# Performance work log

Hardware: AMD Instinct MI355X
Metric: run time of the kernel (lower is better)

## Reference

```python
import jax, jax.numpy as jnp
import numpy as np

EPS = 1e-5

def _ln(x, g, b):
    m = x.mean(-1, keepdims=True)
    v = jnp.var(x, axis=-1, keepdims=True)
    return (x - m) * jax.lax.rsqrt(v + EPS) * g + b

def _conv(x, w, b, stride=1, pad=1):
    y = jax.lax.conv_general_dilated(x, w, (stride, stride), [(pad, pad), (pad, pad)],
                                     dimension_numbers=('NCHW', 'OIHW', 'NCHW'))
    return y + b[None, :, None, None]

def _bn(x, g, b, m, v):
    # inference-mode BatchNorm2d
    inv = jax.lax.rsqrt(v + EPS)
    return (x - m[None, :, None, None]) * (g * inv)[None, :, None, None] + b[None, :, None, None]

def _sru_dir(u0, u1, u2, res, vf, vr, bf, br, reverse):
    # elementwise gated recurrence (SRU v2, identity activation, no dropout)
    def step(c, inp):
        a0, a1, a2, rx = inp
        f = jax.nn.sigmoid(a1 + vf * c + bf)
        c2 = f * c + (1.0 - f) * a0
        r = jax.nn.sigmoid(a2 + vr * c2 + br)
        return c2, r * c2 + (1.0 - r) * rx
    c0 = jnp.zeros_like(u0[0])
    _, hs = jax.lax.scan(step, c0, (u0, u1, u2, res), reverse=reverse)
    return hs

def _sru_layer(x, g, b, wp, w, vc, bias, k, h):
    # x: [L,B,n_in]; layer_norm on input, factored weight (projection), bidirectional
    xn = _ln(x, g, b)
    L, B, _ = xn.shape
    U = (xn @ wp) @ w                      # [L,B,2*k*h]
    U = U.reshape(L, B, 2, k, h)
    outs = []
    for d, rev in ((0, False), (1, True)):
        u = U[:, :, d]
        res = u[..., 3, :] if k == 4 else xn[..., d * h:(d + 1) * h]
        outs.append(_sru_dir(u[..., 0, :], u[..., 1, :], u[..., 2, :], res,
                             vc[d, 0], vc[d, 1], bias[d, 0], bias[d, 1], rev))
    return jnp.concatenate(outs, axis=-1)

def _forward(x, conv0_w, conv0_b, rconv1_w, rconv1_b, rbn1_g, rbn1_b, rbn1_m, rbn1_v,
             rconv2_w, rconv2_b, rbn2_g, rbn2_b, rbn2_m, rbn2_v,
             ln0_g, ln0_b, wproj0, w0, vc0, bias0, ln_g, ln_b, wproj, w, vc, bias,
             cln_g, cln_b, cls_w):
    H = 512
    h = _conv(x, conv0_w, conv0_b, stride=2)           # [B,32,F/2,T/2]
    for i in range(3):                                  # 3 residual blocks
        r = h
        h1 = jax.nn.relu(_bn(_conv(h, rconv1_w[i], rconv1_b[i]), rbn1_g[i], rbn1_b[i], rbn1_m[i], rbn1_v[i]))
        h2 = _bn(_conv(h1, rconv2_w[i], rconv2_b[i]), rbn2_g[i], rbn2_b[i], rbn2_m[i], rbn2_v[i])
        h = jax.nn.relu(h2 + r)
    Bb, C, Fr, Tt = h.shape
    s = h.reshape(Bb, C * Fr, Tt).transpose(2, 0, 1)   # [T,B,2048]
    s = _sru_layer(s, ln0_g, ln0_b, wproj0, w0, vc0, bias0, 4, H)  # layer 0: n_in != n_out -> k=4
    for i in range(3):                                  # layers 1..3: n_in == n_out -> k=3
        s = _sru_layer(s, ln_g[i], ln_b[i], wproj[i], w[i], vc[i], bias[i], 3, H)
    s = s.transpose(1, 0, 2)                            # [B,T,1024]
    s = _ln(s, cln_g, cln_b)
    return s @ cls_w                                    # [B,T,30]

def setup_inputs():
    key = jax.random.key(0)
    ks = iter(jax.random.split(key, 32))
    def nrm(shape, scale=1.0):
        return jax.random.normal(next(ks), shape, jnp.float32) * scale
    H, P, F2, D, hb = 512, 256, 2048, 1024, -2.0
    d = {}
    d['x'] = nrm((16, 1, 128, 2048))
    d['conv0_w'] = nrm((32, 1, 3, 3), (2.0 / 9) ** 0.5)
    d['conv0_b'] = jnp.zeros((32,))
    d['rconv1_w'] = nrm((3, 32, 32, 3, 3), (2.0 / (32 * 9)) ** 0.5)
    d['rconv1_b'] = jnp.zeros((3, 32))
    d['rbn1_g'] = jnp.ones((3, 32)); d['rbn1_b'] = jnp.zeros((3, 32))
    d['rbn1_m'] = nrm((3, 32), 0.1); d['rbn1_v'] = jnp.ones((3, 32))
    d['rconv2_w'] = nrm((3, 32, 32, 3, 3), (2.0 / (32 * 9)) ** 0.5)
    d['rconv2_b'] = jnp.zeros((3, 32))
    d['rbn2_g'] = 0.1 * jnp.ones((3, 32)); d['rbn2_b'] = jnp.zeros((3, 32))
    d['rbn2_m'] = nrm((3, 32), 0.1); d['rbn2_v'] = jnp.ones((3, 32))
    d['ln0_g'] = jnp.ones((F2,)); d['ln0_b'] = jnp.zeros((F2,))
    d['wproj0'] = nrm((F2, P), F2 ** -0.5)
    d['w0'] = nrm((P, 2 * 4 * H), P ** -0.5)
    d['vc0'] = nrm((2, 2, H), 0.1)
    d['bias0'] = jnp.zeros((2, 2, H)).at[:, 0].set(hb)
    d['ln_g'] = jnp.ones((3, D)); d['ln_b'] = jnp.zeros((3, D))
    d['wproj'] = nrm((3, D, P), D ** -0.5)
    d['w'] = nrm((3, P, 2 * 3 * H), P ** -0.5)
    d['vc'] = nrm((3, 2, 2, H), 0.1)
    d['bias'] = jnp.zeros((3, 2, 2, H)).at[:, :, 0].set(hb)
    d['cln_g'] = jnp.ones((D,)); d['cln_b'] = jnp.zeros((D,))
    d['cls_w'] = nrm((D, 30), D ** -0.5)
    return d

def reference(x, conv0_w, conv0_b, rconv1_w, rconv1_b, rbn1_g, rbn1_b, rbn1_m, rbn1_v,
              rconv2_w, rconv2_b, rbn2_g, rbn2_b, rbn2_m, rbn2_v,
              ln0_g, ln0_b, wproj0, w0, vc0, bias0, ln_g, ln_b, wproj, w, vc, bias,
              cln_g, cln_b, cls_w):
    return _forward(x, conv0_w, conv0_b, rconv1_w, rconv1_b, rbn1_g, rbn1_b, rbn1_m, rbn1_v,
                    rconv2_w, rconv2_b, rbn2_g, rbn2_b, rbn2_m, rbn2_v,
                    ln0_g, ln0_b, wproj0, w0, vc0, bias0, ln_g, ln_b, wproj, w, vc, bias,
                    cln_g, cln_b, cls_w)
```

## Files before the change

kernel.cpp:

```cpp
#include <hip/hip_runtime.h>
#include <hip/hip_bf16.h>
#include <math.h>

#define DEV __device__ __forceinline__

typedef __attribute__((ext_vector_type(8))) short short8;
typedef __attribute__((ext_vector_type(4))) float floatx4;

DEV float b2f_lo(unsigned u) { return __uint_as_float(u << 16); }
DEV float b2f_hi(unsigned u) { return __uint_as_float(u & 0xffff0000u); }

#if __has_builtin(__builtin_amdgcn_exp2f)
DEV float fexp2_(float x) { return __builtin_amdgcn_exp2f(x); }
#else
DEV float fexp2_(float x) { return exp2f(x); }
#endif
#if __has_builtin(__builtin_amdgcn_rcpf)
DEV float frcp_(float x) { return __builtin_amdgcn_rcpf(x); }
#else
DEV float frcp_(float x) { return 1.f / x; }
#endif

DEV void gl2lds16(const void* g, void* l) {
  __builtin_amdgcn_global_load_lds(
      (const __attribute__((address_space(1))) unsigned int*)g,
      (__attribute__((address_space(3))) unsigned int*)l, 16, 0, 0);
}

union U8 { uint4 u; __hip_bfloat16 h[8]; };

DEV int swz64(int x)    { return (x & ~63) | ((x & 15) << 2) | ((x >> 4) & 3); }
DEV int invswz64(int x) { return (x & ~63) | ((x & 3) << 4) | ((x >> 2) & 15); }

__global__ __launch_bounds__(256) void conv_stem_nhwc(const float* __restrict__ x,
    const float* __restrict__ w, const float* __restrict__ bias,
    __hip_bfloat16* __restrict__ out) {
  __shared__ float sX[3][2052];
  __shared__ float sW[288];
  __shared__ float sB[32];
  const int tid = threadIdx.x;
  const int f = blockIdx.x, n = blockIdx.y;
  const float* xb = x + (size_t)n * 262144;

  for (int i = tid; i < 1536; i += 256) {
    int r = i >> 9, c4 = i & 511;
    int fi = 2 * f - 1 + r;
    float4 v = {0.f, 0.f, 0.f, 0.f};
    if (fi >= 0 && fi < 128) v = *(const float4*)&xb[fi * 2048 + c4 * 4];
    sX[r][1 + c4 * 4 + 0] = v.x;
    sX[r][1 + c4 * 4 + 1] = v.y;
    sX[r][1 + c4 * 4 + 2] = v.z;
    sX[r][1 + c4 * 4 + 3] = v.w;
  }
  if (tid < 3) { sX[tid][0] = 0.f; sX[tid][2049] = 0.f; }
  for (int i = tid; i < 288; i += 256) sW[i] = w[i];
  if (tid < 32) sB[tid] = bias[tid];
  __syncthreads();

  float xv[4][9];
#pragma unroll
  for (int q = 0; q < 4; ++q) {
    int t = tid + q * 256;
#pragma unroll
    for (int r = 0; r < 3; ++r)
#pragma unroll
      for (int dc = 0; dc < 3; ++dc)
        xv[q][r * 3 + dc] = sX[r][2 * t + dc];
  }

  U8 ores[4][4];
#pragma unroll
  for (int ocq = 0; ocq < 4; ++ocq) {
#pragma unroll
    for (int oo = 0; oo < 8; ++oo) {
      float w9[9];
#pragma unroll
      for (int qq = 0; qq < 9; ++qq) w9[qq] = sW[(ocq * 8 + oo) * 9 + qq];
      float b0 = sB[ocq * 8 + oo];
#pragma unroll
      for (int q = 0; q < 4; ++q) {
        float acc = b0;
#pragma unroll
        for (int qq = 0; qq < 9; ++qq) acc = fmaf(w9[qq], xv[q][qq], acc);
        ores[ocq][q].h[oo] = __float2bfloat16(acc);
      }
    }
  }

#pragma unroll
  for (int q = 0; q < 4; ++q) {
    int t = tid + q * 256;
    uint4* dst = (uint4*)&out[(((size_t)n * 64 + f) * 1024 + t) * 32];
    dst[0] = ores[0][q].u;
    dst[1] = ores[1][q].u;
    dst[2] = ores[2][q].u;
    dst[3] = ores[3][q].u;
  }
}

__global__ __launch_bounds__(256) void wtap_conv6(const float* __restrict__ w1,
    const float* __restrict__ w2, __hip_bfloat16* __restrict__ out) {
  int i = blockIdx.x * 256 + threadIdx.x;
  if (i < 55296) {
    int b = i / 9216, r = i - b * 9216;
    int layer = b >> 1, which = b & 1;
    const float* src = (which ? w2 : w1) + layer * 9216;
    int tap = r >> 10, oc = (r >> 5) & 31, ic = r & 31;
    out[b * 9216 + r] = __float2bfloat16(src[(oc * 32 + ic) * 9 + tap]);
  }
}

template <int ADD>
__global__ __launch_bounds__(256) void conv_mfma(const __hip_bfloat16* __restrict__ Hin,
    const __hip_bfloat16* __restrict__ wt,
    const float* __restrict__ cb, const float* __restrict__ bg,
    const float* __restrict__ bb, const float* __restrict__ bm,
    const float* __restrict__ bv, __hip_bfloat16* Hres) {
  __shared__ __hip_bfloat16 sIn[6 * 66 * 40];
  __hip_bfloat16* sOut = sIn;
  const int tid = threadIdx.x;
  const int tb = blockIdx.x, fb = blockIdx.y, n = blockIdx.z;
  const int t0 = tb * 64, f0 = fb * 4;
  const __hip_bfloat16* Hb = Hin + (size_t)n * 2097152;

  for (int c = tid; c < 1584; c += 256) {
    int rr = c / 264;
    int r2 = c - rr * 264;
    int p = r2 >> 2, icq = r2 & 3;
    int fi = f0 - 1 + rr;
    int tg = t0 + p - 1;
    uint4 v = {0, 0, 0, 0};
    if (fi >= 0 && fi < 64 && tg >= 0 && tg < 1024)
      v = *(const uint4*)&Hb[((size_t)fi * 1024 + tg) * 32 + icq * 8];
    *(uint4*)&sIn[(rr * 66 + p) * 40 + icq * 8] = v;
  }

  const int lane = tid & 63, wave = tid >> 6;
  const int fr = lane & 15, fq = lane >> 4;
  short8 bfrag[9][2];
#pragma unroll
  for (int tap = 0; tap < 9; ++tap)
#pragma unroll
    for (int j = 0; j < 2; ++j)
      bfrag[tap][j] = *(const short8*)&wt[(tap * 32 + j * 16 + fr) * 32 + fq * 8];

  __syncthreads();

  const int tw = wave * 16;
  floatx4 acc[4][2];
#pragma unroll
  for (int fp = 0; fp < 4; ++fp)
#pragma unroll
    for (int j = 0; j < 2; ++j) acc[fp][j] = (floatx4){0.f, 0.f, 0.f, 0.f};

#pragma unroll
  for (int fp = 0; fp < 4; ++fp) {
    int pbase = tw + fr;
#pragma unroll
    for (int df = 0; df < 3; ++df)
#pragma unroll
      for (int dc = 0; dc < 3; ++dc) {
        short8 af =
            *(const short8*)&sIn[((fp + df) * 66 + pbase + dc) * 40 + fq * 8];
        acc[fp][0] = __builtin_amdgcn_mfma_f32_16x16x32_bf16(
            af, bfrag[df * 3 + dc][0], acc[fp][0], 0, 0, 0);
        acc[fp][1] = __builtin_amdgcn_mfma_f32_16x16x32_bf16(
            af, bfrag[df * 3 + dc][1], acc[fp][1], 0, 0, 0);
      }
  }

  float sc0 = bg[fr] * rsqrtf(bv[fr] + 1e-5f);
  float sh0 = (cb[fr] - bm[fr]) * sc0 + bb[fr];
  float sc1 = bg[fr + 16] * rsqrtf(bv[fr + 16] + 1e-5f);
  float sh1 = (cb[fr + 16] - bm[fr + 16]) * sc1 + bb[fr + 16];

  __syncthreads();
#pragma unroll
  for (int fp = 0; fp < 4; ++fp)
#pragma unroll
    for (int j = 0; j < 2; ++j) {
      float sc = j ? sc1 : sc0, sh = j ? sh1 : sh0;
#pragma unroll
      for (int reg = 0; reg < 4; ++reg) {
        int t_l = tw + fq * 4 + reg;
        sOut[(fp * 64 + t_l) * 40 + j * 16 + fr] =
            __float2bfloat16(acc[fp][j][reg] * sc + sh);
      }
    }
  __syncthreads();

  for (int c = tid; c < 1024; c += 256) {
    int fp = c >> 8, rem = c & 255;
    int t_l = rem >> 2, icq = rem & 3;
    U8 y;
    y.u = *(uint4*)&sOut[(fp * 64 + t_l) * 40 + icq * 8];
    size_t addr = (((size_t)n * 64 + f0 + fp) * 1024 + t0 + t_l) * 32 + icq * 8;
    U8 o;
    if (ADD) {
      U8 r;
      r.u = *(const uint4*)&Hres[addr];
#pragma unroll
      for (int i = 0; i < 8; ++i)
        o.h[i] = __float2bfloat16(
            fmaxf(__bfloat162float(y.h[i]) + __bfloat162float(r.h[i]), 0.f));
    } else {
#pragma unroll
      for (int i = 0; i < 8; ++i)
        o.h[i] = __float2bfloat16(fmaxf(__bfloat162float(y.h[i]), 0.f));
    }
    *(uint4*)&Hres[addr] = o.u;
  }
}

__global__ __launch_bounds__(256) void ln_nhwc(const __hip_bfloat16* __restrict__ H,
    const float* __restrict__ g, const float* __restrict__ b,
    __hip_bfloat16* __restrict__ xn) {
  int r = blockIdx.x;
  int t = r >> 4, n = r & 15;
  int tid = threadIdx.x;
  int f = tid >> 2, icq = tid & 3;
  U8 v;
  v.u = *(const uint4*)&H[(((size_t)n * 64 + f) * 1024 + t) * 32 + icq * 8];
  float xv[8];
  float sum = 0.f, ss = 0.f;
#pragma unroll
  for (int i = 0; i < 8; ++i) {
    xv[i] = __bfloat162float(v.h[i]);
    sum += xv[i];
    ss += xv[i] * xv[i];
  }
#pragma unroll
  for (int off = 32; off > 0; off >>= 1) {
    sum += __shfl_down(sum, off);
    ss  += __shfl_down(ss, off);
  }
  __shared__ float red[8];
  int lane = tid & 63, wave = tid >> 6;
  if (lane == 0) { red[wave] = sum; red[4 + wave] = ss; }
  __syncthreads();
  sum = red[0] + red[1] + red[2] + red[3];
  ss  = red[4] + red[5] + red[6] + red[7];
  float mean = sum * (1.f / 2048.f);
  float var = ss * (1.f / 2048.f) - mean * mean;
  float inv = rsqrtf(var + 1e-5f);
  U8 o;
#pragma unroll
  for (int i = 0; i < 8; ++i) {
    int cf = (icq * 8 + i) * 64 + f;
    o.h[i] = __float2bfloat16((xv[i] - mean) * inv * g[cf] + b[cf]);
  }
  *(uint4*)&xn[(size_t)r * 2048 + tid * 8] = o.u;
}

__global__ __launch_bounds__(256) void wt_perm0(const float* __restrict__ in,
    __hip_bfloat16* __restrict__ out) {
  int i = blockIdx.x * 256 + threadIdx.x;
  int p = i >> 11, kp = i & 2047;
  int ic = kp & 31, f = kp >> 5;
  out[i] = __float2bfloat16(in[(ic * 64 + f) * 256 + p]);
}

__global__ __launch_bounds__(256) void wt_bf16(const float* __restrict__ in,
    __hip_bfloat16* __restrict__ out, int K, int N, int inStride, int outStride) {
  __shared__ float tile[32][33];
  int x = threadIdx.x, y0 = threadIdx.y;
  int bn = blockIdx.x * 32;
  int bk = blockIdx.y * 32;
  const float* src = in + (size_t)blockIdx.z * inStride;
  __hip_bfloat16* dst = out + (size_t)blockIdx.z * outStride;
#pragma unroll
  for (int i = 0; i < 4; ++i) {
    int yy = y0 + i * 8;
    tile[yy][x] = src[(size_t)(bk + yy) * N + bn + x];
  }
  __syncthreads();
#pragma unroll
  for (int i = 0; i < 4; ++i) {
    int yy = y0 + i * 8;
    dst[(size_t)(bn + yy) * K + bk + x] = __float2bfloat16(tile[x][yy]);
  }
}

__global__ void wexp_prep(const float* __restrict__ in,
    __hip_bfloat16* __restrict__ out, int korig, int inStride, int outStride) {
  __shared__ float tile[32][33];
  int jt = blockIdx.x;
  int ckt = blockIdx.y;
  int z = blockIdx.z;
  int layer = z >> 3, dk = z & 7;
  int d = dk >> 2, k = dk & 3;
  if (k >= korig) return;
  const float* src = in + (size_t)layer * inStride;
  __hip_bfloat16* dst = out + (size_t)layer * outStride;
  int x = threadIdx.x, y0 = threadIdx.y;
#pragma unroll
  for (int i = 0; i < 4; ++i) {
    int yy = y0 + i * 8;
    tile[yy][x] = src[(size_t)(ckt * 32 + yy) * (korig * 1024) +
                      (d * korig + k) * 512 + jt * 32 + x];
  }
  __syncthreads();
#pragma unroll
  for (int i = 0; i < 4; ++i) {
    int yy = y0 + i * 8;
    int ch = d * 512 + jt * 32 + yy;
    int rOld;
    if (korig == 4)
      rOld = (k < 2) ? (ch * 2 + k) : (2048 + ch * 2 + (k - 2));
    else
      rOld = (k < 2) ? (ch * 2 + k) : (2048 + ch);
    int rNew = invswz64(rOld);
    int ckp = swz64(ckt * 32 + x);
    dst[(size_t)rNew * 256 + ckp] = __float2bfloat16(tile[x][yy]);
  }
}

__global__ __launch_bounds__(256) void colsb_prep(const float* __restrict__ bias0,
    const float* __restrict__ bias3, float2* __restrict__ out) {
  int i = blockIdx.x * 256 + threadIdx.x;
  if (i >= 13312) return;
  const float NL2E = -1.44269504f;
  float s = 1.f, bb = 0.f;
  if (i < 4096) {
    int col = i;
    if (col < 2048) {
      int ch = col >> 1, e = col & 1;
      int d = ch >> 9, jj = ch & 511;
      if (e) { s = NL2E; bb = NL2E * bias0[d * 1024 + jj]; }
    } else {
      int cc = col - 2048, ch = cc >> 1, e = cc & 1;
      int d = ch >> 9, jj = ch & 511;
      if (!e) { s = NL2E; bb = NL2E * bias0[d * 1024 + 512 + jj]; }
    }
  } else {
    int rem = i - 4096;
    int layer = rem / 3072, col = rem - layer * 3072;
    const float* bsrc = bias3 + layer * 2048;
    if (col < 2048) {
      int ch = col >> 1, e = col & 1;
      int d = ch >> 9, jj = ch & 511;
      if (e) { s = NL2E; bb = NL2E * bsrc[d * 1024 + jj]; }
    } else {
      int ch = col - 2048;
      int d = ch >> 9, jj = ch & 511;
      s = NL2E; bb = NL2E * bsrc[d * 1024 + 512 + jj];
    }
  }
  out[i] = make_float2(s, bb);
}

__global__ __launch_bounds__(256) void wct_prep(const float* __restrict__ in,
    __hip_bfloat16* __restrict__ out) {
  int i = blockIdx.x * 256 + threadIdx.x;
  int nn = i >> 10, kk = i & 1023;
  out[i] = __float2bfloat16(nn < 30 ? in[kk * 30 + nn] : 0.f);
}

__global__ __launch_bounds__(256) void gemm_bf16(const __hip_bfloat16* __restrict__ A,
    const __hip_bfloat16* __restrict__ Bt, __hip_bfloat16* __restrict__ C,
    const float2* __restrict__ csb, int M, int N, int K) {
  __shared__ __hip_bfloat16 As[2][128 * 64];
  __shared__ __hip_bfloat16 Bs[2][128 * 64];
  const int tid = threadIdx.x;
  const int gx = gridDim.x;
  const int nwg = gx * gridDim.y;
  const int bid = blockIdx.y * gx + blockIdx.x;
  const int wgid = (bid & 7) * (nwg >> 3) + (bid >> 3);
  const int m0 = (wgid / gx) * 128, n0 = (wgid % gx) * 128;
  const int lane = tid & 63, wave = tid >> 6;
  const int wm = wave & 1, wn = wave >> 1;
  const int fr = lane & 15, fq = lane >> 4;
  const int frx = fr & 7;

  const int srow8 = lane >> 3;
  const int lslot = (lane & 7) ^ srow8;
  const __hip_bfloat16* gaS = &A[(size_t)(m0 + wave * 32 + srow8) * K + lslot * 8];
  const __hip_bfloat16* gbS = &Bt[(size_t)(n0 + wave * 32 + srow8) * K + lslot * 8];

  floatx4 acc[4][4];
#pragma unroll
  for (int i = 0; i < 4; ++i)
#pragma unroll
    for (int j = 0; j < 4; ++j)
      acc[i][j] = (floatx4){0.f, 0.f, 0.f, 0.f};

#define STAGE(BUF, kk)                                                    \
  {                                                                       \
    _Pragma("unroll") for (int i = 0; i < 4; ++i) {                       \
      gl2lds16(gaS + (size_t)i * 8 * K + (kk),                            \
               &As[BUF][(wave * 32 + i * 8) * 64]);                       \
      gl2lds16(gbS + (size_t)i * 8 * K + (kk),                            \
               &Bs[BUF][(wave * 32 + i * 8) * 64]);                       \
    }                                                                     \
  }
#define COMPUTE(BUF)                                                      \
  {                                                                       \
    _Pragma("unroll") for (int s = 0; s < 2; ++s) {                       \
      const int sl = ((s * 4 + fq) ^ frx) * 8;                            \
      short8 af[4], bf_[4];                                               \
      _Pragma("unroll") for (int i = 0; i < 4; ++i) {                     \
        af[i]  = *(const short8*)&As[BUF][(wm * 64 + i * 16 + fr) * 64 + sl]; \
        bf_[i] = *(const short8*)&Bs[BUF][(wn * 64 + i * 16 + fr) * 64 + sl]; \
      }                                                                   \
      _Pragma("unroll") for (int i = 0; i < 4; ++i)                       \
        _Pragma("unroll") for (int j = 0; j < 4; ++j)                     \
          acc[i][j] = __builtin_amdgcn_mfma_f32_16x16x32_bf16(            \
              af[i], bf_[j], acc[i][j], 0, 0, 0);                         \
    }                                                                     \
  }
#define CFENCE asm volatile("" ::: "memory")

  STAGE(0, 0);
  for (int k0 = 0; k0 < K; k0 += 128) {
    STAGE(1, k0 + 64);
    asm volatile("s_waitcnt vmcnt(8)" ::: "memory");
    __builtin_amdgcn_s_barrier();
    COMPUTE(0);
    CFENCE;
    __builtin_amdgcn_s_barrier();
    if (k0 + 128 < K) {
      STAGE(0, k0 + 128);
      asm volatile("s_waitcnt vmcnt(8)" ::: "memory");
    } else {
      asm volatile("s_waitcnt vmcnt(0)" ::: "memory");
    }
    __builtin_amdgcn_s_barrier();
    COMPUTE(1);
    CFENCE;
    __builtin_amdgcn_s_barrier();
  }
#undef STAGE
#undef COMPUTE
#undef CFENCE

  const int p0 = n0 + wn * 64 + fr * 4;
  float s0 = 1.f, s1 = 1.f, s2 = 1.f, s3 = 1.f;
  float c0 = 0.f, c1 = 0.f, c2v = 0.f, c3 = 0.f;
  if (csb) {
    float2 t0 = csb[p0], t1 = csb[p0 + 1], t2 = csb[p0 + 2], t3 = csb[p0 + 3];
    s0 = t0.x; c0 = t0.y; s1 = t1.x; c1 = t1.y;
    s2 = t2.x; c2v = t2.y; s3 = t3.x; c3 = t3.y;
  }
#pragma unroll
  for (int i = 0; i < 4; ++i)
#pragma unroll
    for (int reg = 0; reg < 4; ++reg) {
      int row = m0 + wm * 64 + i * 16 + fq * 4 + reg;
      union { uint2 u; __hip_bfloat16 h[4]; } o;
      o.h[0] = __float2bfloat16(fmaf(acc[i][0][reg], s0, c0));
      o.h[1] = __float2bfloat16(fmaf(acc[i][1][reg], s1, c1));
      o.h[2] = __float2bfloat16(fmaf(acc[i][2][reg], s2, c2v));
      o.h[3] = __float2bfloat16(fmaf(acc[i][3][reg], s3, c3));
      *(uint2*)&C[(size_t)row * N + p0] = o.u;
    }
}

__global__ __launch_bounds__(256) void cls_gemm(const __hip_bfloat16* __restrict__ A,
    const __hip_bfloat16* __restrict__ Wct, float* __restrict__ out) {
  const int tid = threadIdx.x;
  const int lane = tid & 63, wave = tid >> 6;
  const int fr = lane & 15, fq = lane >> 4;
  const int m0 = (blockIdx.x * 4 + wave) * 16;
  floatx4 acc[2];
  acc[0] = (floatx4){0.f, 0.f, 0.f, 0.f};
  acc[1] = (floatx4){0.f, 0.f, 0.f, 0.f};
#pragma unroll 4
  for (int k0 = 0; k0 < 1024; k0 += 32) {
    short8 af = *(const short8*)&A[(size_t)(m0 + fr) * 1024 + k0 + fq * 8];
    short8 b0 = *(const short8*)&Wct[(size_t)fr * 1024 + k0 + fq * 8];
    short8 b1 = *(const short8*)&Wct[(size_t)(16 + fr) * 1024 + k0 + fq * 8];
    acc[0] = __builtin_amdgcn_mfma_f32_16x16x32_bf16(af, b0, acc[0], 0, 0, 0);
    acc[1] = __builtin_amdgcn_mfma_f32_16x16x32_bf16(af, b1, acc[1], 0, 0, 0);
  }
#pragma unroll
  for (int j = 0; j < 2; ++j) {
    int col = j * 16 + fr;
    if (col < 30) {
#pragma unroll
      for (int reg = 0; reg < 4; ++reg) {
        int row = m0 + fq * 4 + reg;
        int t = row >> 4, n = row & 15;
        out[(size_t)n * 30720 + t * 30 + col] = acc[j][reg];
      }
    }
  }
}

template <int ROWB>
__global__ __launch_bounds__(128) void scan_c(const __hip_bfloat16* __restrict__ U,
    const float* __restrict__ vc, __hip_bfloat16* __restrict__ c2out) {
  __shared__ uint slab[16 * 1024];
  const int b = blockIdx.x;
  const int lane = threadIdx.x & 63;
  const int wave = threadIdx.x >> 6;
  const int jb = (b * 64) & 511;
  const int n = (b >> 3) & 15;
  const int d = b >> 7;
  const float NL2E = -1.44269504f;

  const ptrdiff_t US = (ptrdiff_t)16 * ROWB;
  const char* stripe0 = (const char*)U + (size_t)n * ROWB + (size_t)(d * 512 + jb) * 4;
  const char* baseDir = d ? stripe0 + 1023 * US : stripe0;
  const ptrdiff_t stepStride = d ? -US : US;

  if (wave == 1) {
    const int D = 12;
    const int sgrp = lane >> 4;
    const int chunk = lane & 15;
#define ISSUE4(BB)                                                        \
    {                                                                     \
      int slot = (BB) & 15;                                               \
      _Pragma("unroll") for (int i = 0; i < 4; ++i) {                     \
        int s = (BB) * 16 + i * 4 + sgrp;                                 \
        const char* src = baseDir + (ptrdiff_t)s * stepStride + chunk * 16; \
        gl2lds16(src, (char*)slab + slot * 4096 + i * 1024);              \
      }                                                                   \
    }
    for (int bb = 0; bb < D; ++bb) ISSUE4(bb);
    for (int bb = 0; bb < 64; ++bb) {
      if (bb + D < 64) {
        ISSUE4(bb + D);
        asm volatile("s_waitcnt vmcnt(48)" ::: "memory");
      } else {
        asm volatile("s_waitcnt vmcnt(0)" ::: "memory");
      }
      __builtin_amdgcn_s_barrier();
    }
#undef ISSUE4
  } else {
    const int j = jb + lane;
    float vf2 = NL2E * vc[d * 1024 + j];
    char* Ob = (char*)c2out + (size_t)n * 2048 + (size_t)(d * 512 + j) * 2;
    const int OS = d ? -32768 : 32768;
    int ooff = d ? 1023 * 32768 : 0;
    float c = 0.f;
    for (int bb = 0; bb < 64; ++bb) {
      __builtin_amdgcn_s_barrier();
      asm volatile("" ::: "memory");
      const uint* slot = slab + (bb & 15) * 1024;
#pragma unroll
      for (int ss = 0; ss < 16; ++ss) {
        uint u = slot[ss * 64 + lane];
        float a0 = b2f_lo(u), a1p = b2f_hi(u);
        float f = frcp_(1.f + fexp2_(fmaf(vf2, c, a1p)));
        c = fmaf(f, c - a0, a0);
        *(__hip_bfloat16*)(Ob + ooff) = __float2bfloat16(c);
        ooff += OS;
      }
    }
  }
}

template <int K4>
__global__ __launch_bounds__(256) void yln(const __hip_bfloat16* __restrict__ c2buf,
    const __hip_bfloat16* __restrict__ U, const __hip_bfloat16* __restrict__ xn,
    const float* __restrict__ vc, const float* __restrict__ g,
    const float* __restrict__ b, __hip_bfloat16* __restrict__ outx) {
  int r = blockIdx.x;
  int tid = threadIdx.x;
  int ch0 = tid * 4;
  const float NL2E = -1.44269504f;

  union { ushort4 u; __hip_bfloat16 h[4]; } cv;
  cv.u = *(const ushort4*)&c2buf[(size_t)r * 1024 + ch0];
  float a2p[4], rx[4];
  if (K4) {
    uint4 pr = *(const uint4*)((const char*)U + (size_t)r * 8192 + 4096 + tid * 16);
    uint pp[4] = {pr.x, pr.y, pr.z, pr.w};
#pragma unroll
    for (int i = 0; i < 4; ++i) { a2p[i] = b2f_lo(pp[i]); rx[i] = b2f_hi(pp[i]); }
  } else {
    union { ushort4 u; __hip_bfloat16 h[4]; } av, xv;
    av.u = *(const ushort4*)((const char*)U + (size_t)r * 6144 + 4096 + tid * 8);
    xv.u = *(const ushort4*)&xn[(size_t)r * 1024 + ch0];
#pragma unroll
    for (int i = 0; i < 4; ++i) {
      a2p[i] = __bfloat162float(av.h[i]);
      rx[i]  = __bfloat162float(xv.h[i]);
    }
  }

  int d = ch0 >> 9, j0 = ch0 & 511;
  float y[4], sum = 0.f, ss = 0.f;
#pragma unroll
  for (int i = 0; i < 4; ++i) {
    float vr2 = NL2E * vc[d * 1024 + 512 + j0 + i];
    float cc = __bfloat162float(cv.h[i]);
    float rr = frcp_(1.f + fexp2_(fmaf(vr2, cc, a2p[i])));
    y[i] = fmaf(rr, cc - rx[i], rx[i]);
    sum += y[i];
    ss += y[i] * y[i];
  }
#pragma unroll
  for (int off = 32; off > 0; off >>= 1) {
    sum += __shfl_down(sum, off);
    ss  += __shfl_down(ss, off);
  }
  __shared__ float red[8];
  int lane = tid & 63, wave = tid >> 6;
  if (lane == 0) { red[wave] = sum; red[4 + wave] = ss; }
  __syncthreads();
  sum = red[0] + red[1] + red[2] + red[3];
  ss  = red[4] + red[5] + red[6] + red[7];
  float mean = sum * (1.f / 1024.f);
  float var = ss * (1.f / 1024.f) - mean * mean;
  float inv = rsqrtf(var + 1e-5f);
  float4 gv = *(const float4*)&g[ch0];
  float4 bv = *(const float4*)&b[ch0];
  float gg[4] = {gv.x, gv.y, gv.z, gv.w};
  float bb[4] = {bv.x, bv.y, bv.z, bv.w};
  union { ushort4 u; __hip_bfloat16 h[4]; } o;
#pragma unroll
  for (int i = 0; i < 4; ++i)
    o.h[i] = __float2bfloat16((y[i] - mean) * inv * gg[i] + bb[i]);
  *(ushort4*)&outx[(size_t)r * 1024 + ch0] = o.u;
}

extern "C" void kernel_launch(void* const* d_in, const int* in_sizes, int n_in,
                              void* d_out, int out_size, void* d_ws, size_t ws_size,
                              hipStream_t stream) {
  const float* x        = (const float*)d_in[0];
  const float* conv0_w  = (const float*)d_in[1];
  const float* conv0_b  = (const float*)d_in[2];
  const float* rconv1_w = (const float*)d_in[3];
  const float* rconv1_b = (const float*)d_in[4];
  const float* rbn1_g   = (const float*)d_in[5];
  const float* rbn1_b   = (const float*)d_in[6];
  const float* rbn1_m   = (const float*)d_in[7];
  const float* rbn1_v   = (const float*)d_in[8];
  const float* rconv2_w = (const float*)d_in[9];
  const float* rconv2_b = (const float*)d_in[10];
  const float* rbn2_g   = (const float*)d_in[11];
  const float* rbn2_b   = (const float*)d_in[12];
  const float* rbn2_m   = (const float*)d_in[13];
  const float* rbn2_v   = (const float*)d_in[14];
  const float* ln0_g    = (const float*)d_in[15];
  const float* ln0_b    = (const float*)d_in[16];
  const float* wproj0   = (const float*)d_in[17];
  const float* w0       = (const float*)d_in[18];
  const float* vc0      = (const float*)d_in[19];
  const float* bias0    = (const float*)d_in[20];
  const float* ln_g     = (const float*)d_in[21];
  const float* ln_b     = (const float*)d_in[22];
  const float* wproj    = (const float*)d_in[23];
  const float* w        = (const float*)d_in[24];
  const float* vc       = (const float*)d_in[25];
  const float* bias     = (const float*)d_in[26];
  const float* cln_g    = (const float*)d_in[27];
  const float* cln_b    = (const float*)d_in[28];
  const float* cls_w    = (const float*)d_in[29];
  float* out = (float*)d_out;

  float* Af = (float*)d_ws;
  float* Bf = Af + 33554432;
  __hip_bfloat16* Ah = (__hip_bfloat16*)Af;
  __hip_bfloat16* Bh = (__hip_bfloat16*)Bf;

  __hip_bfloat16* hA     = Ah;
  __hip_bfloat16* hB     = Bh;
  __hip_bfloat16* wt_all = Ah + 62914560;
  __hip_bfloat16* Wp0t   = Ah + 52428800;

  __hip_bfloat16* c2   = Bh;
  __hip_bfloat16* xnc  = Bh + 16777216;
  __hip_bfloat16* xn3  = Bh + 33554432;
  __hip_bfloat16* tmp  = Bh + 50331648;
  __hip_bfloat16* W3p  = Bh + 54525952;
  __hip_bfloat16* W0p  = Bh + 57671680;
  __hip_bfloat16* Wpt3 = Bh + 58720256;
  float2* csb          = (float2*)(Bh + 59506688);
  __hip_bfloat16* xn0  = Bh;
  __hip_bfloat16* U    = Ah;
  __hip_bfloat16* Wct  = Ah;

  const float2* csb4 = csb;
  const float2* csb3 = csb + 4096;

  wtap_conv6<<<216, 256, 0, stream>>>(rconv1_w, rconv2_w, wt_all);
  wt_perm0<<<2048, 256, 0, stream>>>(wproj0, Wp0t);
  wexp_prep<<<dim3(16, 8, 8), dim3(32, 8), 0, stream>>>(w0, W0p, 4, 0, 0);
  wexp_prep<<<dim3(16, 8, 24), dim3(32, 8), 0, stream>>>(w, W3p, 3,
                                                         786432, 786432);
  wt_bf16<<<dim3(8, 32, 3), dim3(32, 8), 0, stream>>>(wproj, Wpt3, 1024, 256,
                                                      262144, 262144);
  colsb_prep<<<52, 256, 0, stream>>>(bias0, bias, csb);

  conv_stem_nhwc<<<dim3(64, 16), 256, 0, stream>>>(x, conv0_w, conv0_b, hA);
  for (int i = 0; i < 3; ++i) {
    conv_mfma<0><<<dim3(16, 16, 16), 256, 0, stream>>>(hA, wt_all + (i * 2) * 9216,
        rconv1_b + i * 32, rbn1_g + i * 32, rbn1_b + i * 32,
        rbn1_m + i * 32, rbn1_v + i * 32, hB);
    conv_mfma<1><<<dim3(16, 16, 16), 256, 0, stream>>>(hB, wt_all + (i * 2 + 1) * 9216,
        rconv2_b + i * 32, rbn2_g + i * 32, rbn2_b + i * 32,
        rbn2_m + i * 32, rbn2_v + i * 32, hA);
  }

  ln_nhwc<<<16384, 256, 0, stream>>>(hA, ln0_g, ln0_b, xn0);
  gemm_bf16<<<dim3(2, 128), 256, 0, stream>>>(xn0, Wp0t, tmp, nullptr,
                                              16384, 256, 2048);
  gemm_bf16<<<dim3(32, 128), 256, 0, stream>>>(tmp, W0p, U, csb4,
                                               16384, 4096, 256);
  scan_c<8192><<<256, 128, 0, stream>>>(U, vc0, c2);
  __hip_bfloat16* xnA = xn3;
  __hip_bfloat16* xnB = xnc;
  yln<1><<<16384, 256, 0, stream>>>(c2, U, nullptr, vc0, ln_g, ln_b, xnA);

  for (int i = 0; i < 3; ++i) {
    gemm_bf16<<<dim3(2, 128), 256, 0, stream>>>(xnA, Wpt3 + i * 262144, tmp,
                                                nullptr, 16384, 256, 1024);
    gemm_bf16<<<dim3(24, 128), 256, 0, stream>>>(tmp, W3p + i * 786432, U,
                                                 csb3 + i * 3072, 16384, 3072, 256);
    scan_c<6144><<<256, 128, 0, stream>>>(U, vc + i * 2048, c2);
    const float* gg = (i < 2) ? (ln_g + (i + 1) * 1024) : cln_g;
    const float* bb = (i < 2) ? (ln_b + (i + 1) * 1024) : cln_b;
    yln<0><<<16384, 256, 0, stream>>>(c2, U, xnA, vc + i * 2048, gg, bb, xnB);
    __hip_bfloat16* sw = xnA; xnA = xnB; xnB = sw;
  }

  wct_prep<<<128, 256, 0, stream>>>(cls_w, Wct);
  cls_gemm<<<256, 256, 0, stream>>>(xnA, Wct, out);
}
```

Measured before the change: 966.1 us.

## Fuse both residual-block convolutions into one kernel with halo recompute

```diff
diff --git a/kernel.cpp b/kernel.cpp
--- a/kernel.cpp
+++ b/kernel.cpp
@@ -110,39 +110,97 @@
   }
 }
 
-template <int ADD>
-__global__ __launch_bounds__(256) void conv_mfma(const __hip_bfloat16* __restrict__ Hin,
-    const __hip_bfloat16* __restrict__ wt,
-    const float* __restrict__ cb, const float* __restrict__ bg,
-    const float* __restrict__ bb, const float* __restrict__ bm,
-    const float* __restrict__ bv, __hip_bfloat16* Hres) {
-  __shared__ __hip_bfloat16 sIn[6 * 66 * 40];
-  __hip_bfloat16* sOut = sIn;
+__global__ __launch_bounds__(256) void conv_res_fused(
+    const __hip_bfloat16* __restrict__ Hin,
+    const __hip_bfloat16* __restrict__ wt1, const __hip_bfloat16* __restrict__ wt2,
+    const float* __restrict__ cb1, const float* __restrict__ bg1,
+    const float* __restrict__ bb1, const float* __restrict__ bm1,
+    const float* __restrict__ bv1,
+    const float* __restrict__ cb2, const float* __restrict__ bg2,
+    const float* __restrict__ bb2, const float* __restrict__ bm2,
+    const float* __restrict__ bv2,
+    __hip_bfloat16* __restrict__ Hout) {
+  __shared__ __hip_bfloat16 sIn[8 * 68 * 40];
+  __shared__ __hip_bfloat16 sH1[6 * 66 * 40];
   const int tid = threadIdx.x;
   const int tb = blockIdx.x, fb = blockIdx.y, n = blockIdx.z;
   const int t0 = tb * 64, f0 = fb * 4;
   const __hip_bfloat16* Hb = Hin + (size_t)n * 2097152;
 
-  for (int c = tid; c < 1584; c += 256) {
-    int rr = c / 264;
-    int r2 = c - rr * 264;
+  for (int c = tid; c < 2176; c += 256) {
+    int rr = c / 272;
+    int r2 = c - rr * 272;
     int p = r2 >> 2, icq = r2 & 3;
-    int fi = f0 - 1 + rr;
-    int tg = t0 + p - 1;
+    int fi = f0 - 2 + rr;
+    int tg = t0 + p - 2;
     uint4 v = {0, 0, 0, 0};
     if (fi >= 0 && fi < 64 && tg >= 0 && tg < 1024)
       v = *(const uint4*)&Hb[((size_t)fi * 1024 + tg) * 32 + icq * 8];
-    *(uint4*)&sIn[(rr * 66 + p) * 40 + icq * 8] = v;
+    *(uint4*)&sIn[(rr * 68 + p) * 40 + icq * 8] = v;
   }
 
   const int lane = tid & 63, wave = tid >> 6;
   const int fr = lane & 15, fq = lane >> 4;
+
   short8 bfrag[9][2];
 #pragma unroll
   for (int tap = 0; tap < 9; ++tap)
 #pragma unroll
     for (int j = 0; j < 2; ++j)
-      bfrag[tap][j] = *(const short8*)&wt[(tap * 32 + j * 16 + fr) * 32 + fq * 8];
+      bfrag[tap][j] = *(const short8*)&wt1[(tap * 32 + j * 16 + fr) * 32 + fq * 8];
+  float sc10 = bg1[fr] * rsqrtf(bv1[fr] + 1e-5f);
+  float sh10 = (cb1[fr] - bm1[fr]) * sc10 + bb1[fr];
+  float sc11 = bg1[fr + 16] * rsqrtf(bv1[fr + 16] + 1e-5f);
+  float sh11 = (cb1[fr + 16] - bm1[fr + 16]) * sc11 + bb1[fr + 16];
+
+  __syncthreads();
+
+  {
+    const int tgbase5[5] = {0, 16, 32, 48, 50};
+    for (int u = wave; u < 30; u += 4) {
+      int frow = u / 5;
+      int tg = u - frow * 5;
+      int tb0 = tgbase5[tg];
+      floatx4 a0 = (floatx4){0.f, 0.f, 0.f, 0.f};
+      floatx4 a1 = (floatx4){0.f, 0.f, 0.f, 0.f};
+#pragma unroll
+      for (int df = 0; df < 3; ++df)
+#pragma unroll
+        for (int dc = 0; dc < 3; ++dc) {
+          short8 af = *(const short8*)
+              &sIn[((frow + df) * 68 + tb0 + fr + dc) * 40 + fq * 8];
+          a0 = __builtin_amdgcn_mfma_f32_16x16x32_bf16(
+              af, bfrag[df * 3 + dc][0], a0, 0, 0, 0);
+          a1 = __builtin_amdgcn_mfma_f32_16x16x32_bf16(
+              af, bfrag[df * 3 + dc][1], a1, 0, 0, 0);
+        }
+      int gf = f0 - 1 + frow;
+      bool fv = (gf >= 0) && (gf < 64);
+      __hip_bfloat16 z = __float2bfloat16(0.f);
+#pragma unroll
+      for (int reg = 0; reg < 4; ++reg) {
+        int tl = tb0 + fq * 4 + reg;
+        int gt = t0 - 1 + tl;
+        bool v = fv && (gt >= 0) && (gt < 1024);
+        __hip_bfloat16 h0 = __float2bfloat16(a0[reg] * sc10 + sh10);
+        __hip_bfloat16 h1 = __float2bfloat16(a1[reg] * sc11 + sh11);
+        h0 = __float2bfloat16(fmaxf(__bfloat162float(h0), 0.f));
+        h1 = __float2bfloat16(fmaxf(__bfloat162float(h1), 0.f));
+        sH1[(frow * 66 + tl) * 40 + fr] = v ? h0 : z;
+        sH1[(frow * 66 + tl) * 40 + 16 + fr] = v ? h1 : z;
+      }
+    }
+  }
+
+#pragma unroll
+  for (int tap = 0; tap < 9; ++tap)
+#pragma unroll
+    for (int j = 0; j < 2; ++j)
+      bfrag[tap][j] = *(const short8*)&wt2[(tap * 32 + j * 16 + fr) * 32 + fq * 8];
+  float sc20 = bg2[fr] * rsqrtf(bv2[fr] + 1e-5f);
+  float sh20 = (cb2[fr] - bm2[fr]) * sc20 + bb2[fr];
+  float sc21 = bg2[fr + 16] * rsqrtf(bv2[fr + 16] + 1e-5f);
+  float sh21 = (cb2[fr + 16] - bm2[fr + 16]) * sc21 + bb2[fr + 16];
 
   __syncthreads();
 
@@ -161,7 +219,7 @@
 #pragma unroll
       for (int dc = 0; dc < 3; ++dc) {
         short8 af =
-            *(const short8*)&sIn[((fp + df) * 66 + pbase + dc) * 40 + fq * 8];
+            *(const short8*)&sH1[((fp + df) * 66 + pbase + dc) * 40 + fq * 8];
         acc[fp][0] = __builtin_amdgcn_mfma_f32_16x16x32_bf16(
             af, bfrag[df * 3 + dc][0], acc[fp][0], 0, 0, 0);
         acc[fp][1] = __builtin_amdgcn_mfma_f32_16x16x32_bf16(
@@ -169,21 +227,16 @@
       }
   }
 
-  float sc0 = bg[fr] * rsqrtf(bv[fr] + 1e-5f);
-  float sh0 = (cb[fr] - bm[fr]) * sc0 + bb[fr];
-  float sc1 = bg[fr + 16] * rsqrtf(bv[fr + 16] + 1e-5f);
-  float sh1 = (cb[fr + 16] - bm[fr + 16]) * sc1 + bb[fr + 16];
-
   __syncthreads();
 #pragma unroll
   for (int fp = 0; fp < 4; ++fp)
 #pragma unroll
     for (int j = 0; j < 2; ++j) {
-      float sc = j ? sc1 : sc0, sh = j ? sh1 : sh0;
+      float sc = j ? sc21 : sc20, sh = j ? sh21 : sh20;
 #pragma unroll
       for (int reg = 0; reg < 4; ++reg) {
         int t_l = tw + fq * 4 + reg;
-        sOut[(fp * 64 + t_l) * 40 + j * 16 + fr] =
+        sH1[(fp * 64 + t_l) * 40 + j * 16 + fr] =
             __float2bfloat16(acc[fp][j][reg] * sc + sh);
       }
     }
@@ -193,22 +246,16 @@
     int fp = c >> 8, rem = c & 255;
     int t_l = rem >> 2, icq = rem & 3;
     U8 y;
-    y.u = *(uint4*)&sOut[(fp * 64 + t_l) * 40 + icq * 8];
+    y.u = *(uint4*)&sH1[(fp * 64 + t_l) * 40 + icq * 8];
+    U8 r;
+    r.u = *(uint4*)&sIn[((fp + 2) * 68 + t_l + 2) * 40 + icq * 8];
+    U8 o;
+#pragma unroll
+    for (int i = 0; i < 8; ++i)
+      o.h[i] = __float2bfloat16(
+          fmaxf(__bfloat162float(y.h[i]) + __bfloat162float(r.h[i]), 0.f));
     size_t addr = (((size_t)n * 64 + f0 + fp) * 1024 + t0 + t_l) * 32 + icq * 8;
-    U8 o;
-    if (ADD) {
-      U8 r;
-      r.u = *(const uint4*)&Hres[addr];
-#pragma unroll
-      for (int i = 0; i < 8; ++i)
-        o.h[i] = __float2bfloat16(
-            fmaxf(__bfloat162float(y.h[i]) + __bfloat162float(r.h[i]), 0.f));
-    } else {
-#pragma unroll
-      for (int i = 0; i < 8; ++i)
-        o.h[i] = __float2bfloat16(fmaxf(__bfloat162float(y.h[i]), 0.f));
-    }
-    *(uint4*)&Hres[addr] = o.u;
+    *(uint4*)&Hout[addr] = o.u;
   }
 }
 
@@ -656,10 +703,9 @@
   __hip_bfloat16* Ah = (__hip_bfloat16*)Af;
   __hip_bfloat16* Bh = (__hip_bfloat16*)Bf;
 
-  __hip_bfloat16* hA     = Ah;
-  __hip_bfloat16* hB     = Bh;
-  __hip_bfloat16* wt_all = Ah + 62914560;
-  __hip_bfloat16* Wp0t   = Ah + 52428800;
+  __hip_bfloat16* hA = Ah;
+  __hip_bfloat16* hB = Bh;
+  __hip_bfloat16* hC = Ah + 33554432;
 
   __hip_bfloat16* c2   = Bh;
   __hip_bfloat16* xnc  = Bh + 16777216;
@@ -669,6 +715,8 @@
   __hip_bfloat16* W0p  = Bh + 57671680;
   __hip_bfloat16* Wpt3 = Bh + 58720256;
   float2* csb          = (float2*)(Bh + 59506688);
+  __hip_bfloat16* wt_all = Bh + 59768832;
+  __hip_bfloat16* Wp0t   = Bh + 60293120;
   __hip_bfloat16* xn0  = Bh;
   __hip_bfloat16* U    = Ah;
   __hip_bfloat16* Wct  = Ah;
@@ -686,13 +734,14 @@
   colsb_prep<<<52, 256, 0, stream>>>(bias0, bias, csb);
 
   conv_stem_nhwc<<<dim3(64, 16), 256, 0, stream>>>(x, conv0_w, conv0_b, hA);
+  __hip_bfloat16* rs[4] = {hA, hB, hC, hA};
   for (int i = 0; i < 3; ++i) {
-    conv_mfma<0><<<dim3(16, 16, 16), 256, 0, stream>>>(hA, wt_all + (i * 2) * 9216,
+    conv_res_fused<<<dim3(16, 16, 16), 256, 0, stream>>>(rs[i],
+        wt_all + (i * 2) * 9216, wt_all + (i * 2 + 1) * 9216,
         rconv1_b + i * 32, rbn1_g + i * 32, rbn1_b + i * 32,
-        rbn1_m + i * 32, rbn1_v + i * 32, hB);
-    conv_mfma<1><<<dim3(16, 16, 16), 256, 0, stream>>>(hB, wt_all + (i * 2 + 1) * 9216,
+        rbn1_m + i * 32, rbn1_v + i * 32,
         rconv2_b + i * 32, rbn2_g + i * 32, rbn2_b + i * 32,
-        rbn2_m + i * 32, rbn2_v + i * 32, hA);
+        rbn2_m + i * 32, rbn2_v + i * 32, rs[i + 1]);
   }
 
   ln_nhwc<<<16384, 256, 0, stream>>>(hA, ln0_g, ln0_b, xn0);
```

New measurement: 1.031 ms. 6.7% more time.
